# Performance work log

Hardware: AMD Instinct MI355X
Metric: run time of the kernel (lower is better)

## Reference

```python
import jax, jax.numpy as jnp
import numpy as np

B = 4            # num sequences
Q_LEN = 512      # new query tokens per sequence
KV_LEN = 2048    # total kv context per sequence
PAST = KV_LEN - Q_LEN
N_QO, N_KV, HEAD = 32, 8, 128
BS = 16          # page / block size
BLOCKS_PER_SEQ = KV_LEN // BS
NUM_BLOCKS = B * BLOCKS_PER_SEQ


def setup_inputs() -> dict:
    key = jax.random.key(0)
    k1, k2, k3, k4, k5 = jax.random.split(key, 5)
    n_tokens = B * Q_LEN
    query = jax.random.normal(k1, (n_tokens, N_QO * HEAD), dtype=jnp.float32)
    key_t = jax.random.normal(k2, (n_tokens, N_KV * HEAD), dtype=jnp.float32)
    value_t = jax.random.normal(k3, (n_tokens, N_KV * HEAD), dtype=jnp.float32)
    key_cache = jax.random.normal(k4, (NUM_BLOCKS, BS, N_KV, HEAD), dtype=jnp.float32)
    value_cache = jax.random.normal(k5, (NUM_BLOCKS, BS, N_KV, HEAD), dtype=jnp.float32)
    # block tables: a permutation of all blocks (each seq owns disjoint, shuffled pages)
    rng = np.random.default_rng(0)
    bt = rng.permutation(NUM_BLOCKS).reshape(B, BLOCKS_PER_SEQ).astype(np.int32)
    # slot indices (into flattened [num_blocks*block_size] token space) for the new tokens
    pos = np.arange(PAST, KV_LEN)                        # positions of new tokens in each seq
    slots = bt[:, pos // BS] * BS + (pos % BS)           # [B, Q_LEN]
    return {
        'query': query,
        'key': key_t,
        'value': value_t,
        'key_cache': key_cache,
        'value_cache': value_cache,
        'block_tables': jnp.asarray(bt),
        'new_cache_slots': jnp.asarray(slots.reshape(-1), dtype=jnp.int32),
    }


def reference(query, key, value, key_cache, value_cache, block_tables, new_cache_slots):
    n_tokens = query.shape[0]
    num_blocks, bs, n_kv, d = key_cache.shape
    b, blocks_per_seq = block_tables.shape
    q_len = n_tokens // b
    kv_len = blocks_per_seq * bs
    n_qo = query.shape[1] // d
    g = n_qo // n_kv  # GQA group size

    q = query.reshape(b, q_len, n_qo, d).astype(jnp.float32)
    k_new = key.reshape(n_tokens, n_kv, d)
    v_new = value.reshape(n_tokens, n_kv, d)

    # write new k/v into the paged cache at their slots (set_kv_cache)
    kc = key_cache.reshape(num_blocks * bs, n_kv, d).at[new_cache_slots].set(k_new)
    vc = value_cache.reshape(num_blocks * bs, n_kv, d).at[new_cache_slots].set(v_new)

    # per-sequence paged gather: token t of seq i lives at block_tables[i, t//bs]*bs + t%bs
    tok_idx = (block_tables[:, :, None] * bs + jnp.arange(bs, dtype=block_tables.dtype)).reshape(b, kv_len)
    k = kc[tok_idx].astype(jnp.float32)  # [b, kv_len, n_kv, d]
    v = vc[tok_idx].astype(jnp.float32)

    # GQA: query head (h*g + j) attends with kv head h (== repeat_interleave on kv heads)
    qg = q.reshape(b, q_len, n_kv, g, d)
    sm_scale = 1.0 / jnp.sqrt(jnp.float32(d))
    scores = jnp.einsum('bqhgd,bkhd->bhgqk', qg, k) * sm_scale  # [b, n_kv, g, q, kv]

    # causal mask with offset: mask where k_idx - q_idx > kv_len - q_len
    q_idx = jnp.arange(q_len)
    k_idx = jnp.arange(kv_len)
    mask = (k_idx[None, :] - q_idx[:, None]) > (kv_len - q_len)  # [q, kv]
    scores = jnp.where(mask, -jnp.inf, scores)

    p = jax.nn.softmax(scores, axis=-1)
    o = jnp.einsum('bhgqk,bkhd->bqhgd', p, v)  # [b, q, n_kv, g, d]
    return o.reshape(n_tokens, n_qo * d).astype(query.dtype)
```

## Files before the change

kernel.cpp:

```cpp
#include <hip/hip_runtime.h>
#include <hip/hip_bf16.h>

#define BQ    4
#define QL    512
#define KVL   2048
#define PASTN 1536
#define NKV   8
#define DH    128
#define BPS   128

typedef __bf16 bf16x8 __attribute__((ext_vector_type(8)));
typedef float  f32x4  __attribute__((ext_vector_type(4)));
typedef float  f32x16 __attribute__((ext_vector_type(16)));

#if __has_builtin(__builtin_amdgcn_exp2f)
#define EXP2F(x) __builtin_amdgcn_exp2f(x)
#else
#define EXP2F(x) exp2f(x)
#endif

__device__ __forceinline__ unsigned short f32_to_bf16(float f) {
    unsigned u = __builtin_bit_cast(unsigned, f);
    u += 0x7fffu + ((u >> 16) & 1u);
    return (unsigned short)(u >> 16);
}

__device__ __forceinline__ unsigned pk_bf16(float a, float b) {
    return (unsigned)f32_to_bf16(a) | ((unsigned)f32_to_bf16(b) << 16);
}

__device__ __forceinline__ unsigned pk_trunc(float lo, float hi) {
    return __builtin_amdgcn_perm(__builtin_bit_cast(unsigned, hi),
                                 __builtin_bit_cast(unsigned, lo), 0x07060302u);
}

__device__ __forceinline__ void load_lds16(const unsigned short* g, unsigned short* l) {
    __builtin_amdgcn_global_load_lds(
        (const __attribute__((address_space(1))) void*)g,
        (__attribute__((address_space(3))) void*)l, 16, 0, 0);
}

__device__ __forceinline__ void swap32(unsigned &x, unsigned &y) {
    asm("v_permlane32_swap_b32 %0, %1" : "+v"(x), "+v"(y));
}

__device__ __forceinline__ void lacc_add(float &L, unsigned p) {
    L += __builtin_bit_cast(float, p << 16);
    L += __builtin_bit_cast(float, p & 0xffff0000u);
}

__global__ __launch_bounds__(256) void gather_k_kernel(
    const float* __restrict__ key, const float* __restrict__ key_cache,
    const int* __restrict__ bt, unsigned short* __restrict__ Kb)
{
  const int gidx = blockIdx.x * 256 + threadIdx.x;
  const int d  = (gidx & 31) * 4;
  const int p  = (gidx >> 5) & (KVL - 1);
  const int bh = gidx >> 16;
  const int hh = bh & 7;
  const int bb = bh >> 3;
  const float* src;
  if (p < PASTN) {
    const int blk = bt[bb * BPS + (p >> 4)];
    src = key_cache + (size_t)((blk * 16 + (p & 15)) * 8 + hh) * DH + d;
  } else {
    src = key + (size_t)((bb * QL + (p - PASTN)) * 8 + hh) * DH + d;
  }
  const float4 v = *(const float4*)src;
  uint2 o;
  o.x = pk_bf16(v.x, v.y);
  o.y = pk_bf16(v.z, v.w);
  *(uint2*)(Kb + ((size_t)bh * KVL + p) * DH + d) = o;
}

#define VLS 132
__global__ __launch_bounds__(256) void gather_vt_kernel(
    const float* __restrict__ value, const float* __restrict__ value_cache,
    const int* __restrict__ bt, unsigned short* __restrict__ VTb)
{
  __shared__ unsigned short Vl[64 * VLS];
  const int t   = blockIdx.x & 31;
  const int hh  = (blockIdx.x >> 5) & 7;
  const int bb  = blockIdx.x >> 8;
  const int tid = threadIdx.x;
  const int dl  = (tid & 31) * 4;
  const int p0  = tid >> 5;
#pragma unroll
  for (int it = 0; it < 8; ++it) {
    const int pl = p0 + it * 8;
    const int gp = t * 64 + pl;
    const float* src;
    if (gp < PASTN) {
      const int blk = bt[bb * BPS + (gp >> 4)];
      src = value_cache + (size_t)((blk * 16 + (gp & 15)) * 8 + hh) * DH + dl;
    } else {
      src = value + (size_t)((bb * QL + (gp - PASTN)) * 8 + hh) * DH + dl;
    }
    const float4 v = *(const float4*)src;
    uint2 o;
    o.x = pk_bf16(v.x, v.y);
    o.y = pk_bf16(v.z, v.w);
    *(uint2*)&Vl[pl * VLS + dl] = o;
  }
  __syncthreads();
#pragma unroll
  for (int it = 0; it < 4; ++it) {
    const int slot = it * 256 + tid;
    const int d    = slot >> 3;
    const int kv0  = (slot & 7) * 8;
    unsigned rr[4];
#pragma unroll
    for (int i = 0; i < 4; ++i) {
      const unsigned lo = Vl[(kv0 + 2 * i) * VLS + d];
      const unsigned hi = Vl[(kv0 + 2 * i + 1) * VLS + d];
      rr[i] = lo | (hi << 16);
    }
    *(uint4*)(VTb + ((size_t)(bb * 8 + hh) * DH + d) * KVL + t * 64 + kv0) =
        make_uint4(rr[0], rr[1], rr[2], rr[3]);
  }
}

__global__ __launch_bounds__(256, 2) void attn_kernel(
    const float* __restrict__ query,
    const unsigned short* __restrict__ Kb,
    const unsigned short* __restrict__ VTb,
    float* __restrict__ out)
{
  __shared__ unsigned short Klds[2][64 * 128];
  __shared__ unsigned short Vtlds[2][128 * 64];

  const int tid  = threadIdx.x;
  const int w    = tid >> 6;
  const int lane = tid & 63;
  const int cq   = lane & 31;
  const int hi   = lane >> 5;
  const int xk   = cq & 7;

  const int gid = blockIdx.x;
  const int qb  = gid >> 5;
  const int bh  = gid & 31;
  const int b   = bh >> 3;
  const int h   = bh & 7;
  const int q0  = qb * 32;
  const int n_tiles = ((PASTN + q0 + 31) >> 6) + 1;
  const int lim = PASTN + q0 - 64 * (n_tiles - 1);
  const int hq  = h * 4 + w;

  const int kx = lane >> 4;
  const int ku = lane & 15;
  const unsigned short* kgp[4];
#pragma unroll
  for (int i = 0; i < 4; ++i) {
    const int row = 16 * w + 4 * i + kx;
    kgp[i] = Kb + ((size_t)bh * KVL + row) * DH + (ku ^ (row & 7)) * 8;
  }
  const int vx = lane >> 3;
  const int vu = lane & 7;
  const unsigned short* vgp[4];
#pragma unroll
  for (int i = 0; i < 4; ++i) {
    const int row = 32 * w + 8 * i + vx;
    vgp[i] = VTb + ((size_t)bh * DH + row) * KVL + (vu ^ vx) * 8;
  }

  auto issue_tile = [&](int buf) {
#pragma unroll
    for (int i = 0; i < 4; ++i)
      load_lds16(kgp[i], &Klds[buf][2048 * w + 512 * i]);
#pragma unroll
    for (int i = 0; i < 4; ++i)
      load_lds16(vgp[i], &Vtlds[buf][2048 * w + 512 * i]);
#pragma unroll
    for (int i = 0; i < 4; ++i) { kgp[i] += 64 * DH; vgp[i] += 64; }
  };

  issue_tile(0);

  const float qscale = 0.08838834764831845f * 1.4426950408889634f;

  bf16x8 qf[8];
  {
    const float* qp = query + (size_t)(b * QL + q0 + cq) * 4096 + hq * DH + 8 * hi;
#pragma unroll
    for (int ks = 0; ks < 8; ++ks) {
      float4 x = *(const float4*)(qp + 16 * ks);
      float4 y = *(const float4*)(qp + 16 * ks + 4);
      uint4 u;
      u.x = pk_bf16(x.x * qscale, x.y * qscale);
      u.y = pk_bf16(x.z * qscale, x.w * qscale);
      u.z = pk_bf16(y.x * qscale, y.y * qscale);
      u.w = pk_bf16(y.z * qscale, y.w * qscale);
      qf[ks] = __builtin_bit_cast(bf16x8, u);
    }
  }

  f32x16 Oacc[4];
#pragma unroll
  for (int dt = 0; dt < 4; ++dt)
#pragma unroll
    for (int i = 0; i < 16; ++i) Oacc[dt][i] = 0.f;
  float Ls = 0.f;

  for (int t = 0; t < n_tiles; ++t) {
    const int buf = t & 1;
    __syncthreads();
    if (t + 1 < n_tiles) issue_tile(buf ^ 1);

    f32x16 S0, S1;
#pragma unroll
    for (int i = 0; i < 16; ++i) { S0[i] = 0.f; S1[i] = 0.f; }
#pragma unroll
    for (int ks = 0; ks < 8; ++ks) {
      const bf16x8 a0 = __builtin_bit_cast(bf16x8,
          *(const uint4*)&Klds[buf][(cq)      * 128 + 8 * ((2 * ks + hi) ^ xk)]);
      const bf16x8 a1 = __builtin_bit_cast(bf16x8,
          *(const uint4*)&Klds[buf][(32 + cq) * 128 + 8 * ((2 * ks + hi) ^ xk)]);
      S0 = __builtin_amdgcn_mfma_f32_32x32x16_bf16(a0, qf[ks], S0, 0, 0, 0);
      S1 = __builtin_amdgcn_mfma_f32_32x32x16_bf16(a1, qf[ks], S1, 0, 0, 0);
    }

    if (t == n_tiles - 1) {
#pragma unroll
      for (int reg = 0; reg < 16; ++reg) {
        const int rr = (reg & 3) + 8 * (reg >> 2) + 4 * hi;
        if (rr - cq > lim)      S0[reg] = -1e30f;
        if (32 + rr - cq > lim) S1[reg] = -1e30f;
      }
    }

    auto do_half = [&](const f32x16 &S, int kvt) {
#pragma unroll
      for (int s = 0; s < 2; ++s) {
        unsigned p01 = pk_trunc(EXP2F(S[8 * s + 0]), EXP2F(S[8 * s + 1]));
        unsigned p23 = pk_trunc(EXP2F(S[8 * s + 2]), EXP2F(S[8 * s + 3]));
        unsigned q01 = pk_trunc(EXP2F(S[8 * s + 4]), EXP2F(S[8 * s + 5]));
        unsigned q23 = pk_trunc(EXP2F(S[8 * s + 6]), EXP2F(S[8 * s + 7]));
        lacc_add(Ls, p01); lacc_add(Ls, p23);
        lacc_add(Ls, q01); lacc_add(Ls, q23);
        swap32(p01, q01);
        swap32(p23, q23);
        uint4 u; u.x = p01; u.y = p23; u.z = q01; u.w = q23;
        const bf16x8 pf = __builtin_bit_cast(bf16x8, u);
        const int ss = 2 * kvt + s;
#pragma unroll
        for (int dt = 0; dt < 4; ++dt) {
          const bf16x8 vf = __builtin_bit_cast(bf16x8,
              *(const uint4*)&Vtlds[buf][(32 * dt + cq) * 64 + 8 * ((2 * ss + hi) ^ xk)]);
          Oacc[dt] = __builtin_amdgcn_mfma_f32_32x32x16_bf16(vf, pf, Oacc[dt], 0, 0, 0);
        }
      }
    };
    do_half(S0, 0);
    do_half(S1, 1);
  }

  {
    const float other = __shfl_xor(Ls, 32, 64);
    const float inv = 1.0f / (Ls + other);
    float* op = out + (size_t)(b * QL + q0 + cq) * 4096 + hq * DH + 4 * hi;
#pragma unroll
    for (int dt = 0; dt < 4; ++dt) {
#pragma unroll
      for (int rq = 0; rq < 4; ++rq) {
        float4 o4;
        o4.x = Oacc[dt][4 * rq + 0] * inv;
        o4.y = Oacc[dt][4 * rq + 1] * inv;
        o4.z = Oacc[dt][4 * rq + 2] * inv;
        o4.w = Oacc[dt][4 * rq + 3] * inv;
        *(float4*)(op + 32 * dt + 8 * rq) = o4;
      }
    }
  }
}

extern "C" void kernel_launch(void* const* d_in, const int* in_sizes, int n_in,
                              void* d_out, int out_size, void* d_ws, size_t ws_size,
                              hipStream_t stream) {
  const float* query = (const float*)d_in[0];
  const float* key   = (const float*)d_in[1];
  const float* value = (const float*)d_in[2];
  const float* kc    = (const float*)d_in[3];
  const float* vc    = (const float*)d_in[4];
  const int*   bt    = (const int*)d_in[5];
  float* out = (float*)d_out;

  unsigned short* Kb  = (unsigned short*)d_ws;
  unsigned short* VTb = Kb + (size_t)32 * KVL * DH;

  gather_k_kernel<<<8192, 256, 0, stream>>>(key, kc, bt, Kb);
  gather_vt_kernel<<<1024, 256, 0, stream>>>(value, vc, bt, VTb);
  attn_kernel<<<512, 256, 0, stream>>>(query, Kb, VTb, out);
}
```

Before: 229.4 us.

## Fuse K and V gather kernels and strengthen LDS XOR swizzle

Merges the K gather and V-transpose gather into one launch, with blocks below 8192 handling K and the rest handling V, which removes one kernel launch and the serialization between them. The V staging pitch changes from 132 to 130 with split 4-byte LDS writes, aimed at reducing bank conflicts in the transpose. The attention kernel's K/Vt LDS swizzle key now also mixes in row bits 3-4, intended to spread ds_read_b128 accesses across more banks. Producer addressing and consumer reads are changed together, so the layout stays consistent.

```diff
diff --git a/kernel.cpp b/kernel.cpp
--- a/kernel.cpp
+++ b/kernel.cpp
@@ -49,74 +49,74 @@
     L += __builtin_bit_cast(float, p & 0xffff0000u);
 }
 
-__global__ __launch_bounds__(256) void gather_k_kernel(
+#define VLS 130
+__global__ __launch_bounds__(256) void gather_kv_kernel(
     const float* __restrict__ key, const float* __restrict__ key_cache,
-    const int* __restrict__ bt, unsigned short* __restrict__ Kb)
-{
-  const int gidx = blockIdx.x * 256 + threadIdx.x;
-  const int d  = (gidx & 31) * 4;
-  const int p  = (gidx >> 5) & (KVL - 1);
-  const int bh = gidx >> 16;
-  const int hh = bh & 7;
-  const int bb = bh >> 3;
-  const float* src;
-  if (p < PASTN) {
-    const int blk = bt[bb * BPS + (p >> 4)];
-    src = key_cache + (size_t)((blk * 16 + (p & 15)) * 8 + hh) * DH + d;
-  } else {
-    src = key + (size_t)((bb * QL + (p - PASTN)) * 8 + hh) * DH + d;
-  }
-  const float4 v = *(const float4*)src;
-  uint2 o;
-  o.x = pk_bf16(v.x, v.y);
-  o.y = pk_bf16(v.z, v.w);
-  *(uint2*)(Kb + ((size_t)bh * KVL + p) * DH + d) = o;
-}
-
-#define VLS 132
-__global__ __launch_bounds__(256) void gather_vt_kernel(
     const float* __restrict__ value, const float* __restrict__ value_cache,
-    const int* __restrict__ bt, unsigned short* __restrict__ VTb)
+    const int* __restrict__ bt, unsigned short* __restrict__ Kb,
+    unsigned short* __restrict__ VTb)
 {
   __shared__ unsigned short Vl[64 * VLS];
-  const int t   = blockIdx.x & 31;
-  const int hh  = (blockIdx.x >> 5) & 7;
-  const int bb  = blockIdx.x >> 8;
-  const int tid = threadIdx.x;
-  const int dl  = (tid & 31) * 4;
-  const int p0  = tid >> 5;
-#pragma unroll
-  for (int it = 0; it < 8; ++it) {
-    const int pl = p0 + it * 8;
-    const int gp = t * 64 + pl;
+  const int bid = blockIdx.x;
+  if (bid < 8192) {
+    const int gidx = bid * 256 + threadIdx.x;
+    const int d  = (gidx & 31) * 4;
+    const int p  = (gidx >> 5) & (KVL - 1);
+    const int bh = gidx >> 16;
+    const int hh = bh & 7;
+    const int bb = bh >> 3;
     const float* src;
-    if (gp < PASTN) {
-      const int blk = bt[bb * BPS + (gp >> 4)];
-      src = value_cache + (size_t)((blk * 16 + (gp & 15)) * 8 + hh) * DH + dl;
+    if (p < PASTN) {
+      const int blk = bt[bb * BPS + (p >> 4)];
+      src = key_cache + (size_t)((blk * 16 + (p & 15)) * 8 + hh) * DH + d;
     } else {
-      src = value + (size_t)((bb * QL + (gp - PASTN)) * 8 + hh) * DH + dl;
+      src = key + (size_t)((bb * QL + (p - PASTN)) * 8 + hh) * DH + d;
     }
     const float4 v = *(const float4*)src;
     uint2 o;
     o.x = pk_bf16(v.x, v.y);
     o.y = pk_bf16(v.z, v.w);
-    *(uint2*)&Vl[pl * VLS + dl] = o;
-  }
-  __syncthreads();
-#pragma unroll
-  for (int it = 0; it < 4; ++it) {
-    const int slot = it * 256 + tid;
-    const int d    = slot >> 3;
-    const int kv0  = (slot & 7) * 8;
-    unsigned rr[4];
-#pragma unroll
-    for (int i = 0; i < 4; ++i) {
-      const unsigned lo = Vl[(kv0 + 2 * i) * VLS + d];
-      const unsigned hi = Vl[(kv0 + 2 * i + 1) * VLS + d];
-      rr[i] = lo | (hi << 16);
-    }
-    *(uint4*)(VTb + ((size_t)(bb * 8 + hh) * DH + d) * KVL + t * 64 + kv0) =
-        make_uint4(rr[0], rr[1], rr[2], rr[3]);
+    *(uint2*)(Kb + ((size_t)bh * KVL + p) * DH + d) = o;
+  } else {
+    const int vbid = bid - 8192;
+    const int t   = vbid & 31;
+    const int hh  = (vbid >> 5) & 7;
+    const int bb  = vbid >> 8;
+    const int tid = threadIdx.x;
+    const int dl  = (tid & 31) * 4;
+    const int p0  = tid >> 5;
+#pragma unroll
+    for (int it = 0; it < 8; ++it) {
+      const int pl = p0 + it * 8;
+      const int gp = t * 64 + pl;
+      const float* src;
+      if (gp < PASTN) {
+        const int blk = bt[bb * BPS + (gp >> 4)];
+        src = value_cache + (size_t)((blk * 16 + (gp & 15)) * 8 + hh) * DH + dl;
+      } else {
+        src = value + (size_t)((bb * QL + (gp - PASTN)) * 8 + hh) * DH + dl;
+      }
+      const float4 v = *(const float4*)src;
+      unsigned short* dst = &Vl[pl * VLS + dl];
+      *(unsigned*)(dst)     = pk_bf16(v.x, v.y);
+      *(unsigned*)(dst + 2) = pk_bf16(v.z, v.w);
+    }
+    __syncthreads();
+#pragma unroll
+    for (int it = 0; it < 4; ++it) {
+      const int slot = it * 256 + tid;
+      const int d    = slot >> 3;
+      const int kv0  = (slot & 7) * 8;
+      unsigned rr[4];
+#pragma unroll
+      for (int i = 0; i < 4; ++i) {
+        const unsigned lo = Vl[(kv0 + 2 * i) * VLS + d];
+        const unsigned hi = Vl[(kv0 + 2 * i + 1) * VLS + d];
+        rr[i] = lo | (hi << 16);
+      }
+      *(uint4*)(VTb + ((size_t)(bb * 8 + hh) * DH + d) * KVL + t * 64 + kv0) =
+          make_uint4(rr[0], rr[1], rr[2], rr[3]);
+    }
   }
 }
 
@@ -134,7 +134,7 @@
   const int lane = tid & 63;
   const int cq   = lane & 31;
   const int hi   = lane >> 5;
-  const int xk   = cq & 7;
+  const int xkey = (cq & 7) ^ ((cq >> 3) & 3);
 
   const int gid = blockIdx.x;
   const int qb  = gid >> 5;
@@ -152,7 +152,8 @@
 #pragma unroll
   for (int i = 0; i < 4; ++i) {
     const int row = 16 * w + 4 * i + kx;
-    kgp[i] = Kb + ((size_t)bh * KVL + row) * DH + (ku ^ (row & 7)) * 8;
+    const int key = (row & 7) ^ ((row >> 3) & 3);
+    kgp[i] = Kb + ((size_t)bh * KVL + row) * DH + (ku ^ key) * 8;
   }
   const int vx = lane >> 3;
   const int vu = lane & 7;
@@ -160,7 +161,8 @@
 #pragma unroll
   for (int i = 0; i < 4; ++i) {
     const int row = 32 * w + 8 * i + vx;
-    vgp[i] = VTb + ((size_t)bh * DH + row) * KVL + (vu ^ vx) * 8;
+    const int key = (row & 7) ^ ((row >> 3) & 3);
+    vgp[i] = VTb + ((size_t)bh * DH + row) * KVL + (vu ^ key) * 8;
   }
 
   auto issue_tile = [&](int buf) {
@@ -212,9 +214,9 @@
 #pragma unroll
     for (int ks = 0; ks < 8; ++ks) {
       const bf16x8 a0 = __builtin_bit_cast(bf16x8,
-          *(const uint4*)&Klds[buf][(cq)      * 128 + 8 * ((2 * ks + hi) ^ xk)]);
+          *(const uint4*)&Klds[buf][(cq)      * 128 + 8 * ((2 * ks + hi) ^ xkey)]);
       const bf16x8 a1 = __builtin_bit_cast(bf16x8,
-          *(const uint4*)&Klds[buf][(32 + cq) * 128 + 8 * ((2 * ks + hi) ^ xk)]);
+          *(const uint4*)&Klds[buf][(32 + cq) * 128 + 8 * ((2 * ks + hi) ^ xkey)]);
       S0 = __builtin_amdgcn_mfma_f32_32x32x16_bf16(a0, qf[ks], S0, 0, 0, 0);
       S1 = __builtin_amdgcn_mfma_f32_32x32x16_bf16(a1, qf[ks], S1, 0, 0, 0);
     }
@@ -245,7 +247,7 @@
 #pragma unroll
         for (int dt = 0; dt < 4; ++dt) {
           const bf16x8 vf = __builtin_bit_cast(bf16x8,
-              *(const uint4*)&Vtlds[buf][(32 * dt + cq) * 64 + 8 * ((2 * ss + hi) ^ xk)]);
+              *(const uint4*)&Vtlds[buf][(32 * dt + cq) * 64 + 8 * ((2 * ss + hi) ^ xkey)]);
           Oacc[dt] = __builtin_amdgcn_mfma_f32_32x32x16_bf16(vf, pf, Oacc[dt], 0, 0, 0);
         }
       }
@@ -287,7 +289,6 @@
   unsigned short* Kb  = (unsigned short*)d_ws;
   unsigned short* VTb = Kb + (size_t)32 * KVL * DH;
 
-  gather_k_kernel<<<8192, 256, 0, stream>>>(key, kc, bt, Kb);
-  gather_vt_kernel<<<1024, 256, 0, stream>>>(value, vc, bt, VTb);
+  gather_kv_kernel<<<9216, 256, 0, stream>>>(key, kc, value, vc, bt, Kb, VTb);
   attn_kernel<<<512, 256, 0, stream>>>(query, Kb, VTb, out);
 }
```

After: 228.5 us. Within noise of the previous version (-0.4%).
